# Kernel tuning notes

Measured on AMD Instinct MI355X. Metric: run time of the kernel, lower is better.

Reference implementation:

```python
import jax, jax.numpy as jnp
import numpy as np
from jax import lax

B, H, E = 32, 2050, 128        # batch, input height, num_emb (conv width)
N = 2048                        # num_nodes = H - (kernel_size - 1)
C = 128                         # hidden_channels_CNN[0]
G1, G2 = 128, 128               # hidden_channels_GNN
MLP = 100                       # hidden_channels_MLP
OUT = 1                         # output_dim
KS = 3                          # kernel_size
NE = 32768                      # num edges


def setup_inputs() -> dict:
    key = jax.random.key(0)
    ks = jax.random.split(key, 12)
    s = 0.02
    inp = {
        "x": jax.random.normal(ks[0], (B, H, E), dtype=jnp.float32),
        "edge_index": jax.random.randint(ks[1], (2, NE), 0, N, dtype=jnp.int64),
        # Conv2d(1, C, kernel=(KS, E)) -> OIHW weight [C, 1, KS, E]
        "conv_w": jax.random.normal(ks[2], (C, 1, KS, E), dtype=jnp.float32) * s,
        "conv_b": jax.random.normal(ks[3], (C,), dtype=jnp.float32) * s,
        # GCNConv weights (linear has no bias; bias added after aggregation)
        "gW1": jax.random.normal(ks[4], (C, G1), dtype=jnp.float32) * s,
        "gb1": jax.random.normal(ks[5], (G1,), dtype=jnp.float32) * s,
        "gW2": jax.random.normal(ks[6], (G1, G2), dtype=jnp.float32) * s,
        "gb2": jax.random.normal(ks[7], (G2,), dtype=jnp.float32) * s,
        "W1": jax.random.normal(ks[8], (G2 * N, MLP), dtype=jnp.float32) * s,
        "b1": jax.random.normal(ks[9], (MLP,), dtype=jnp.float32) * s,
        "W2": jax.random.normal(ks[10], (MLP, OUT), dtype=jnp.float32) * s,
        "b2": jax.random.normal(ks[11], (OUT,), dtype=jnp.float32) * s,
    }
    return inp


def _gcn_norm(edge_index, n):
    # PyG gcn_norm with add_self_loops=True, edge_weight = 1
    loops = jnp.arange(n, dtype=edge_index.dtype)
    src = jnp.concatenate([edge_index[0], loops])
    dst = jnp.concatenate([edge_index[1], loops])
    deg = jax.ops.segment_sum(jnp.ones_like(dst, dtype=jnp.float32), dst, num_segments=n)
    dinv = jnp.where(deg > 0, lax.rsqrt(jnp.maximum(deg, 1.0)), 0.0)
    norm = dinv[src] * dinv[dst]
    return src, dst, norm


def _gcn_layer(h, src, dst, norm, W, b):
    # h: [B, N, Fin] -> out[b, dst] = sum_e norm_e * (h @ W)[b, src_e] + b
    hw = h @ W                                   # [B, N, Fout]
    msgs = hw[:, src, :] * norm[None, :, None]    # [B, E+N, Fout]
    agg = jnp.zeros_like(hw).at[:, dst, :].add(msgs)
    return agg + b


def reference(x, edge_index, conv_w, conv_b, gW1, gb1, gW2, gb2, W1, b1, W2, b2):
    # CNN feature extraction: [B,1,H,E] conv (KS,E) -> [B,C,N,1]
    x4 = x[:, None, :, :]
    h = lax.conv_general_dilated(x4, conv_w, window_strides=(1, 1), padding='VALID',
                                 dimension_numbers=('NCHW', 'OIHW', 'NCHW'))
    h = jax.nn.relu(h + conv_b[None, :, None, None])
    h = jnp.transpose(h[:, :, :, 0], (0, 2, 1))   # [B, N, C]

    src, dst, norm = _gcn_norm(edge_index, N)
    h = jax.nn.relu(_gcn_layer(h, src, dst, norm, gW1, gb1))
    h = jax.nn.relu(_gcn_layer(h, src, dst, norm, gW2, gb2))

    h = h.reshape(B, -1)                          # [B, N*G2]
    h = jax.nn.relu(h @ W1 + b1)
    # dropout: eval mode (identity)
    out = h @ W2 + b2
    return out.astype(jnp.float32)
```

## Files before the change

### kernel.cpp

```cpp
#include <hip/hip_runtime.h>
#include <stdint.h>

typedef unsigned short u16;
typedef __attribute__((ext_vector_type(8))) short bf16x8;
typedef __attribute__((ext_vector_type(4))) float f32x4;

#define NN 2048
#define NEDGE 32768
#define NBLK 1024
#define KC 256
#define NRG 4
#define PW 112

__device__ __forceinline__ float bf2f(uint32_t u) {
  union { uint32_t i; float f; } c; c.i = u << 16; return c.f;
}
__device__ __forceinline__ uint32_t f2bf(float f) {
  union { float f; uint32_t i; } c; c.f = f;
  uint32_t x = c.i;
  return (x + 0x7fffu + ((x >> 16) & 1u)) >> 16;
}

__device__ __forceinline__ void fma8(float* acc, uint4 q, float wv) {
  acc[0] += wv * bf2f(q.x & 0xffffu);
  acc[1] += wv * bf2f(q.x >> 16);
  acc[2] += wv * bf2f(q.y & 0xffffu);
  acc[3] += wv * bf2f(q.y >> 16);
  acc[4] += wv * bf2f(q.z & 0xffffu);
  acc[5] += wv * bf2f(q.z >> 16);
  acc[6] += wv * bf2f(q.w & 0xffffu);
  acc[7] += wv * bf2f(q.w >> 16);
}

__global__ void k_prep(const float4* __restrict__ cw, uint2* __restrict__ wtb,
                       const float* __restrict__ g1, const float* __restrict__ g2,
                       u16* __restrict__ o1, u16* __restrict__ o2,
                       int* __restrict__ cnt, int* __restrict__ cursor) {
  int blk = blockIdx.x;
  if (blk < 48) {
    int i = blk * 256 + threadIdx.x;
    float4 v = cw[i];
    uint2 o;
    o.x = f2bf(v.x) | (f2bf(v.y) << 16);
    o.y = f2bf(v.z) | (f2bf(v.w) << 16);
    wtb[i] = o;
  } else if (blk < 112) {
    int i = (blk - 48) * 256 + threadIdx.x;
    int r = i >> 7, c = i & 127;
    o1[i] = (u16)f2bf(g1[c * 128 + r]);
    o2[i] = (u16)f2bf(g2[c * 128 + r]);
  } else {
    int i = (blk - 112) * 256 + threadIdx.x;
    cnt[i] = 1; cursor[i] = 0;
  }
}

__global__ void k_count(const int* __restrict__ edge, int* __restrict__ cnt) {
  int i = blockIdx.x * 256 + threadIdx.x;
  if (i < NEDGE) atomicAdd(&cnt[edge[NEDGE + i]], 1);
}

__global__ __launch_bounds__(1024) void k_scan(const int* __restrict__ cnt, int* __restrict__ rowp) {
  __shared__ int s[1024];
  int t = threadIdx.x;
  int c0 = cnt[2 * t], c1 = cnt[2 * t + 1];
  s[t] = c0 + c1;
  __syncthreads();
  for (int off = 1; off < 1024; off <<= 1) {
    int v = (t >= off) ? s[t - off] : 0;
    __syncthreads();
    s[t] += v;
    __syncthreads();
  }
  int excl = s[t] - c0 - c1;
  rowp[2 * t] = excl;
  rowp[2 * t + 1] = excl + c0;
  if (t == 1023) rowp[2048] = s[t];
}

__global__ void k_fill(const int* __restrict__ edge, const int* __restrict__ cnt,
                       const int* __restrict__ rowp, int* __restrict__ cursor,
                       int* __restrict__ colx, float* __restrict__ wgt) {
  int i = blockIdx.x * 256 + threadIdx.x;
  if (i >= NEDGE + NN) return;
  int s, d;
  if (i < NEDGE) { s = edge[i]; d = edge[NEDGE + i]; }
  else { s = i - NEDGE; d = s; }
  float wv = rsqrtf((float)cnt[s] * (float)cnt[d]);
  int pos = atomicAdd(&cursor[d], 1);
  int idx = rowp[d] + pos;
  colx[idx] = s;
  wgt[idx] = wv;
}

__global__ __launch_bounds__(256) void k_gemmf(
    const float* __restrict__ A, const u16* __restrict__ Bt,
    const float* __restrict__ bias, u16* __restrict__ C,
    int K, int bExtra)
{
  __shared__ u16 lA[128 * 64];
  __shared__ u16 lB[128 * 64];
  const int t = threadIdx.x;
  const int Mbase = blockIdx.x * 128;
  const size_t aBase = (size_t)Mbase * 128 + (size_t)(Mbase >> 11) * bExtra;
  const int w = t >> 6, l = t & 63;
  const int wrM = (w >> 1) * 64, wrN = (w & 1) * 64;
  const int lm = l & 15, lkh = l >> 4;
  const int rph0 = t >> 3, pc = t & 7;
  const int rt2 = t >> 1, hf = t & 1;
  f32x4 acc[4][4];
#pragma unroll
  for (int i = 0; i < 4; ++i)
#pragma unroll
    for (int j = 0; j < 4; ++j)
      acc[i][j] = (f32x4){0.f, 0.f, 0.f, 0.f};

  for (int kc = 0; kc < K; kc += 64) {
    __syncthreads();
#pragma unroll
    for (int it = 0; it < 4; ++it) {
      int r = it * 32 + rph0;
      int lc = pc ^ (r & 7);
      char* dstB = (char*)lB + it * 4096 + w * 1024;
      __builtin_amdgcn_global_load_lds(
          (const void*)(Bt + (size_t)r * K + kc + lc * 8), dstB, 16, 0, 0);
    }
    {
      const float4* src = (const float4*)(A + aBase + (size_t)rt2 * 128 + kc + hf * 32);
      float4 f[8];
#pragma unroll
      for (int c = 0; c < 8; ++c) f[c] = src[c];
#pragma unroll
      for (int cc = 0; cc < 4; ++cc) {
        uint4 pk;
        pk.x = f2bf(f[2 * cc].x)     | (f2bf(f[2 * cc].y) << 16);
        pk.y = f2bf(f[2 * cc].z)     | (f2bf(f[2 * cc].w) << 16);
        pk.z = f2bf(f[2 * cc + 1].x) | (f2bf(f[2 * cc + 1].y) << 16);
        pk.w = f2bf(f[2 * cc + 1].z) | (f2bf(f[2 * cc + 1].w) << 16);
        int ch = hf * 4 + cc;
        *(uint4*)((char*)lA + rt2 * 128 + ((ch ^ (rt2 & 7)) << 4)) = pk;
      }
    }
    __syncthreads();
#pragma unroll
    for (int kk = 0; kk < 2; ++kk) {
      int lc = kk * 4 + lkh;
      bf16x8 af[4], bfr[4];
#pragma unroll
      for (int i = 0; i < 4; ++i) {
        int R = wrM + i * 16 + lm;
        af[i] = *(const bf16x8*)((const char*)lA + R * 128 + ((lc ^ (R & 7)) << 4));
      }
#pragma unroll
      for (int j = 0; j < 4; ++j) {
        int R = wrN + j * 16 + lm;
        bfr[j] = *(const bf16x8*)((const char*)lB + R * 128 + ((lc ^ (R & 7)) << 4));
      }
#pragma unroll
      for (int i = 0; i < 4; ++i)
#pragma unroll
        for (int j = 0; j < 4; ++j)
          acc[i][j] = __builtin_amdgcn_mfma_f32_16x16x32_bf16(af[i], bfr[j], acc[i][j], 0, 0, 0);
    }
  }
  const int rq = (l >> 4) * 4;
#pragma unroll
  for (int i = 0; i < 4; ++i) {
#pragma unroll
    for (int j = 0; j < 4; ++j) {
      int col = wrN + j * 16 + lm;
      float bv = bias[col];
#pragma unroll
      for (int q = 0; q < 4; ++q) {
        int g = Mbase + wrM + i * 16 + rq + q;
        int orow = ((g & 2047) << 5) | (g >> 11);
        float v = acc[i][j][q] + bv;
        v = fmaxf(v, 0.f);
        C[(size_t)orow * 128 + col] = (u16)f2bf(v);
      }
    }
  }
}

__global__ __launch_bounds__(256) void k_gemm(
    const u16* __restrict__ A, const u16* __restrict__ Bt,
    const float* __restrict__ bias, u16* __restrict__ C,
    int K)
{
  __shared__ u16 lA[128 * 64];
  __shared__ u16 lB[128 * 64];
  const int t = threadIdx.x;
  const int Mbase = blockIdx.x * 128;
  const size_t aBase = (size_t)Mbase * 128;
  const int w = t >> 6, l = t & 63;
  const int wrM = (w >> 1) * 64, wrN = (w & 1) * 64;
  const int lm = l & 15, lkh = l >> 4;
  const int rph0 = t >> 3, pc = t & 7;
  f32x4 acc[4][4];
#pragma unroll
  for (int i = 0; i < 4; ++i)
#pragma unroll
    for (int j = 0; j < 4; ++j)
      acc[i][j] = (f32x4){0.f, 0.f, 0.f, 0.f};

  for (int kc = 0; kc < K; kc += 64) {
    __syncthreads();
#pragma unroll
    for (int it = 0; it < 4; ++it) {
      int r = it * 32 + rph0;
      int lc = pc ^ (r & 7);
      char* dstA = (char*)lA + it * 4096 + w * 1024;
      char* dstB = (char*)lB + it * 4096 + w * 1024;
      __builtin_amdgcn_global_load_lds(
          (const void*)(A + aBase + (size_t)r * 128 + kc + lc * 8), dstA, 16, 0, 0);
      __builtin_amdgcn_global_load_lds(
          (const void*)(Bt + (size_t)r * K + kc + lc * 8), dstB, 16, 0, 0);
    }
    __syncthreads();
#pragma unroll
    for (int kk = 0; kk < 2; ++kk) {
      int lc = kk * 4 + lkh;
      bf16x8 af[4], bfr[4];
#pragma unroll
      for (int i = 0; i < 4; ++i) {
        int R = wrM + i * 16 + lm;
        af[i] = *(const bf16x8*)((const char*)lA + R * 128 + ((lc ^ (R & 7)) << 4));
      }
#pragma unroll
      for (int j = 0; j < 4; ++j) {
        int R = wrN + j * 16 + lm;
        bfr[j] = *(const bf16x8*)((const char*)lB + R * 128 + ((lc ^ (R & 7)) << 4));
      }
#pragma unroll
      for (int i = 0; i < 4; ++i)
#pragma unroll
        for (int j = 0; j < 4; ++j)
          acc[i][j] = __builtin_amdgcn_mfma_f32_16x16x32_bf16(af[i], bfr[j], acc[i][j], 0, 0, 0);
    }
  }
  const int rq = (l >> 4) * 4;
#pragma unroll
  for (int i = 0; i < 4; ++i) {
#pragma unroll
    for (int j = 0; j < 4; ++j) {
      int col = wrN + j * 16 + lm;
      float bv = bias[col];
#pragma unroll
      for (int q = 0; q < 4; ++q) {
        int row = Mbase + wrM + i * 16 + rq + q;
        float v = acc[i][j][q] + bv;
        v = fmaxf(v, 0.f);
        C[(size_t)row * 128 + col] = (u16)f2bf(v);
      }
    }
  }
}

__global__ __launch_bounds__(256) void k_gatherT(
    const u16* __restrict__ h, const int* __restrict__ rowp,
    const int* __restrict__ colx, const float* __restrict__ wgt,
    u16* __restrict__ out)
{
  const int t = threadIdx.x;
  const int v = blockIdx.x;
  const int b = t >> 3, cg = t & 7;
  const int e0 = rowp[v], e1 = rowp[v + 1];
  float acc[16];
#pragma unroll
  for (int i = 0; i < 16; ++i) acc[i] = 0.f;
  int e = e0;
  for (; e + 2 <= e1; e += 2) {
    int u0 = colx[e], u1 = colx[e + 1];
    float w0 = wgt[e], w1 = wgt[e + 1];
    const uint4* p0 = (const uint4*)(h + ((size_t)u0 * 32 + b) * 128 + cg * 16);
    const uint4* p1 = (const uint4*)(h + ((size_t)u1 * 32 + b) * 128 + cg * 16);
    uint4 qa0 = p0[0], qa1 = p0[1];
    uint4 qb0 = p1[0], qb1 = p1[1];
    fma8(acc, qa0, w0);
    fma8(acc + 8, qa1, w0);
    fma8(acc, qb0, w1);
    fma8(acc + 8, qb1, w1);
  }
  for (; e < e1; ++e) {
    int u = colx[e];
    float wv = wgt[e];
    const uint4* p = (const uint4*)(h + ((size_t)u * 32 + b) * 128 + cg * 16);
    uint4 q0 = p[0], q1 = p[1];
    fma8(acc, q0, wv);
    fma8(acc + 8, q1, wv);
  }
  uint4 o0, o1;
  o0.x = f2bf(acc[0])  | (f2bf(acc[1])  << 16);
  o0.y = f2bf(acc[2])  | (f2bf(acc[3])  << 16);
  o0.z = f2bf(acc[4])  | (f2bf(acc[5])  << 16);
  o0.w = f2bf(acc[6])  | (f2bf(acc[7])  << 16);
  o1.x = f2bf(acc[8])  | (f2bf(acc[9])  << 16);
  o1.y = f2bf(acc[10]) | (f2bf(acc[11]) << 16);
  o1.z = f2bf(acc[12]) | (f2bf(acc[13]) << 16);
  o1.w = f2bf(acc[14]) | (f2bf(acc[15]) << 16);
  uint4* dst = (uint4*)(out + ((size_t)v * 32 + b) * 128 + cg * 16);
  dst[0] = o0;
  dst[1] = o1;
}

__global__ __launch_bounds__(256) void k_mlp1(
    const u16* __restrict__ h3, const float* __restrict__ W1, float* __restrict__ part)
{
  __shared__ u16 sA[32][264];
  __shared__ u16 sB[112][264];
  const int t = threadIdx.x;
  const int blk = blockIdx.x;
  const int j0 = blk * KC;
  {
    int r = t >> 3, q = t & 7;
    int v = (j0 >> 7) + (q >> 2);
    int d = (q & 3) * 32;
    const u16* src = h3 + ((size_t)v * 32 + r) * 128 + d;
#pragma unroll
    for (int u = 0; u < 4; ++u)
      *(bf16x8*)&sA[r][q * 32 + u * 8] = *(const bf16x8*)(src + u * 8);
  }
  for (int it = 0; it < 13; ++it) {
    int task = it * 256 + t;
    if (task < 3200) {
      int jp = task / 25, mq = task % 25;
      const float* wp = W1 + (size_t)(j0 + 2 * jp) * 100 + mq * 4;
      float4 fa = *(const float4*)wp;
      float4 fb = *(const float4*)(wp + 100);
      uint32_t p0 = f2bf(fa.x) | (f2bf(fb.x) << 16);
      uint32_t p1 = f2bf(fa.y) | (f2bf(fb.y) << 16);
      uint32_t p2 = f2bf(fa.z) | (f2bf(fb.z) << 16);
      uint32_t p3 = f2bf(fa.w) | (f2bf(fb.w) << 16);
      int m = mq * 4;
      *(uint32_t*)&sB[m + 0][2 * jp] = p0;
      *(uint32_t*)&sB[m + 1][2 * jp] = p1;
      *(uint32_t*)&sB[m + 2][2 * jp] = p2;
      *(uint32_t*)&sB[m + 3][2 * jp] = p3;
    }
  }
  __syncthreads();
  const int w = t >> 6, l = t & 63;
  const int mt = w >> 1, nh = w & 1;
  const int nt0 = nh * 4, ntn = nh ? 3 : 4;
  const int lm = l & 15, lk8 = (l >> 4) * 8;
  f32x4 acc[4];
#pragma unroll
  for (int n = 0; n < 4; ++n) acc[n] = (f32x4){0.f, 0.f, 0.f, 0.f};
#pragma unroll
  for (int kk = 0; kk < 8; ++kk) {
    int ko = kk * 32 + lk8;
    bf16x8 af = *(const bf16x8*)&sA[mt * 16 + lm][ko];
#pragma unroll
    for (int n = 0; n < 4; ++n) {
      if (n < ntn) {
        bf16x8 bfr = *(const bf16x8*)&sB[(nt0 + n) * 16 + lm][ko];
        acc[n] = __builtin_amdgcn_mfma_f32_16x16x32_bf16(af, bfr, acc[n], 0, 0, 0);
      }
    }
  }
  const int rq = (l >> 4) * 4;
#pragma unroll
  for (int n = 0; n < 4; ++n) {
    if (n < ntn) {
      int m = (nt0 + n) * 16 + lm;
#pragma unroll
      for (int q = 0; q < 4; ++q) {
        int b = mt * 16 + rq + q;
        part[((size_t)blk * 32 + b) * PW + m] = acc[n][q];
      }
    }
  }
}

__global__ __launch_bounds__(256) void k_red(
    const float* __restrict__ part, float* __restrict__ part2)
{
  int e = blockIdx.x * 256 + threadIdx.x;
  int rg = blockIdx.y;
  const float* p = part + (size_t)rg * 256 * (32 * PW) + e;
  float s0 = 0.f, s1 = 0.f, s2 = 0.f, s3 = 0.f;
  for (int r = 0; r < 256; r += 4) {
    s0 += p[(size_t)(r + 0) * (32 * PW)];
    s1 += p[(size_t)(r + 1) * (32 * PW)];
    s2 += p[(size_t)(r + 2) * (32 * PW)];
    s3 += p[(size_t)(r + 3) * (32 * PW)];
  }
  part2[rg * (32 * PW) + e] = (s0 + s1) + (s2 + s3);
}

__global__ __launch_bounds__(128) void k_mlp2(
    const float* __restrict__ part2, const float* __restrict__ b1,
    const float* __restrict__ W2, const float* __restrict__ b2, float* __restrict__ out)
{
  __shared__ float sh[100];
  int b = blockIdx.x, t = threadIdx.x;
  if (t < 100) {
    float s = 0.f;
#pragma unroll
    for (int rg = 0; rg < NRG; ++rg)
      s += part2[rg * (32 * PW) + b * PW + t];
    float h = fmaxf(s + b1[t], 0.f);
    sh[t] = h * W2[t];
  }
  __syncthreads();
  if (t == 0) {
    float s = 0.f;
    for (int m = 0; m < 100; ++m) s += sh[m];
    out[b] = s + b2[0];
  }
}

extern "C" void kernel_launch(void* const* d_in, const int* in_sizes, int n_in,
                              void* d_out, int out_size, void* d_ws, size_t ws_size,
                              hipStream_t stream) {
  (void)in_sizes; (void)n_in; (void)out_size; (void)ws_size;
  const float* x      = (const float*)d_in[0];
  const int* edge     = (const int*)d_in[1];
  const float* conv_w = (const float*)d_in[2];
  const float* conv_b = (const float*)d_in[3];
  const float* gW1    = (const float*)d_in[4];
  const float* gb1    = (const float*)d_in[5];
  const float* gW2    = (const float*)d_in[6];
  const float* gb2    = (const float*)d_in[7];
  const float* W1     = (const float*)d_in[8];
  const float* b1     = (const float*)d_in[9];
  const float* W2     = (const float*)d_in[10];
  const float* b2     = (const float*)d_in[11];
  float* out = (float*)d_out;

  char* ws = (char*)d_ws;
  size_t off = 0;
  auto alloc = [&](size_t bytes) {
    void* p = ws + off;
    off = (off + bytes + 255) & ~(size_t)255;
    return p;
  };
  u16* bufA   = (u16*)alloc(8388608ull * 2);
  u16* bufB   = (u16*)alloc(8388608ull * 2);
  u16* Wtb    = (u16*)alloc(49152ull * 2);
  u16* g1t    = (u16*)alloc(16384ull * 2);
  u16* g2t    = (u16*)alloc(16384ull * 2);
  int* cnt    = (int*)alloc(2048 * 4);
  int* cursor = (int*)alloc(2048 * 4);
  int* rowp   = (int*)alloc(2052 * 4);
  int* colx   = (int*)alloc(34816 * 4);
  float* wgt  = (float*)alloc(34816 * 4);
  float* part = (float*)alloc((size_t)NBLK * 32 * PW * 4);
  float* part2= (float*)alloc((size_t)NRG * (32 * PW) * 4);

  k_prep<<<120, 256, 0, stream>>>((const float4*)conv_w, (uint2*)Wtb,
                                  gW1, gW2, g1t, g2t, cnt, cursor);
  k_count<<<128, 256, 0, stream>>>(edge, cnt);
  k_scan<<<1, 1024, 0, stream>>>(cnt, rowp);
  k_fill<<<(NEDGE + NN + 255) / 256, 256, 0, stream>>>(edge, cnt, rowp, cursor, colx, wgt);

  k_gemmf<<<512, 256, 0, stream>>>(x, Wtb, conv_b, bufA, 384, 256);
  k_gatherT<<<2048, 256, 0, stream>>>(bufA, rowp, colx, wgt, bufB);
  k_gemm<<<512, 256, 0, stream>>>(bufB, g1t, gb1, bufA, 128);
  k_gatherT<<<2048, 256, 0, stream>>>(bufA, rowp, colx, wgt, bufB);
  k_gemm<<<512, 256, 0, stream>>>(bufB, g2t, gb2, bufA, 128);
  k_mlp1<<<NBLK, 256, 0, stream>>>(bufA, W1, part);
  k_red<<<dim3(14, NRG), 256, 0, stream>>>(part, part2);
  k_mlp2<<<32, 128, 0, stream>>>(part2, b1, W2, b2, out);
}
```

Before: 189.6 us.

## Fuse CSR construction into one cooperative kernel and convert weights inside GEMMs

Four small graph-preprocessing kernels (init, degree count, scan, fill) become a single cooperative kernel that separates its phases with grid-wide syncs. The separate weight-prep kernel is removed: the conv and GCN GEMMs now read fp32 weights directly, then convert and transpose them to bf16 in LDS on every tile. This saves several kernel launches. In exchange, every GEMM block repeats the weight conversion, and the cooperative launch plus grid syncs add their own latency.

```diff
diff --git a/kernel.cpp b/kernel.cpp
--- a/kernel.cpp
+++ b/kernel.cpp
@@ -1,5 +1,8 @@
 #include <hip/hip_runtime.h>
+#include <hip/hip_cooperative_groups.h>
 #include <stdint.h>
+
+namespace cg = cooperative_groups;
 
 typedef unsigned short u16;
 typedef __attribute__((ext_vector_type(8))) short bf16x8;
@@ -32,69 +35,56 @@
   acc[7] += wv * bf2f(q.w >> 16);
 }
 
-__global__ void k_prep(const float4* __restrict__ cw, uint2* __restrict__ wtb,
-                       const float* __restrict__ g1, const float* __restrict__ g2,
-                       u16* __restrict__ o1, u16* __restrict__ o2,
-                       int* __restrict__ cnt, int* __restrict__ cursor) {
-  int blk = blockIdx.x;
-  if (blk < 48) {
-    int i = blk * 256 + threadIdx.x;
-    float4 v = cw[i];
-    uint2 o;
-    o.x = f2bf(v.x) | (f2bf(v.y) << 16);
-    o.y = f2bf(v.z) | (f2bf(v.w) << 16);
-    wtb[i] = o;
-  } else if (blk < 112) {
-    int i = (blk - 48) * 256 + threadIdx.x;
-    int r = i >> 7, c = i & 127;
-    o1[i] = (u16)f2bf(g1[c * 128 + r]);
-    o2[i] = (u16)f2bf(g2[c * 128 + r]);
-  } else {
-    int i = (blk - 112) * 256 + threadIdx.x;
-    cnt[i] = 1; cursor[i] = 0;
-  }
-}
-
-__global__ void k_count(const int* __restrict__ edge, int* __restrict__ cnt) {
-  int i = blockIdx.x * 256 + threadIdx.x;
-  if (i < NEDGE) atomicAdd(&cnt[edge[NEDGE + i]], 1);
-}
-
-__global__ __launch_bounds__(1024) void k_scan(const int* __restrict__ cnt, int* __restrict__ rowp) {
-  __shared__ int s[1024];
-  int t = threadIdx.x;
-  int c0 = cnt[2 * t], c1 = cnt[2 * t + 1];
-  s[t] = c0 + c1;
-  __syncthreads();
-  for (int off = 1; off < 1024; off <<= 1) {
-    int v = (t >= off) ? s[t - off] : 0;
+__global__ __launch_bounds__(256) void k_csrc(
+    const int* __restrict__ edge, int* __restrict__ cnt, int* __restrict__ cursor,
+    int* __restrict__ rowp, int* __restrict__ colx, float* __restrict__ wgt)
+{
+  cg::grid_group grid = cg::this_grid();
+  const int gtid = blockIdx.x * 256 + threadIdx.x;
+  if (gtid < NN) { cnt[gtid] = 1; cursor[gtid] = 0; }
+  grid.sync();
+  atomicAdd(&cnt[edge[NEDGE + gtid]], 1);
+  grid.sync();
+  if (blockIdx.x == 0) {
+    __shared__ int s[256];
+    int t = threadIdx.x;
+    int base = t * 8;
+    int c[8]; int sum = 0;
+#pragma unroll
+    for (int i = 0; i < 8; ++i) { c[i] = cnt[base + i]; sum += c[i]; }
+    s[t] = sum;
     __syncthreads();
-    s[t] += v;
-    __syncthreads();
-  }
-  int excl = s[t] - c0 - c1;
-  rowp[2 * t] = excl;
-  rowp[2 * t + 1] = excl + c0;
-  if (t == 1023) rowp[2048] = s[t];
-}
-
-__global__ void k_fill(const int* __restrict__ edge, const int* __restrict__ cnt,
-                       const int* __restrict__ rowp, int* __restrict__ cursor,
-                       int* __restrict__ colx, float* __restrict__ wgt) {
-  int i = blockIdx.x * 256 + threadIdx.x;
-  if (i >= NEDGE + NN) return;
-  int s, d;
-  if (i < NEDGE) { s = edge[i]; d = edge[NEDGE + i]; }
-  else { s = i - NEDGE; d = s; }
-  float wv = rsqrtf((float)cnt[s] * (float)cnt[d]);
-  int pos = atomicAdd(&cursor[d], 1);
-  int idx = rowp[d] + pos;
-  colx[idx] = s;
-  wgt[idx] = wv;
+    for (int off = 1; off < 256; off <<= 1) {
+      int v = (t >= off) ? s[t - off] : 0;
+      __syncthreads();
+      s[t] += v;
+      __syncthreads();
+    }
+    int excl = s[t] - sum;
+#pragma unroll
+    for (int i = 0; i < 8; ++i) { rowp[base + i] = excl; excl += c[i]; }
+    if (t == 255) rowp[2048] = excl;
+  }
+  grid.sync();
+  {
+    int sV = edge[gtid], d = edge[NEDGE + gtid];
+    float wv = rsqrtf((float)cnt[sV] * (float)cnt[d]);
+    int pos = atomicAdd(&cursor[d], 1);
+    int idx = rowp[d] + pos;
+    colx[idx] = sV;
+    wgt[idx] = wv;
+    if (gtid < NN) {
+      float wv2 = rsqrtf((float)cnt[gtid] * (float)cnt[gtid]);
+      int pos2 = atomicAdd(&cursor[gtid], 1);
+      int idx2 = rowp[gtid] + pos2;
+      colx[idx2] = gtid;
+      wgt[idx2] = wv2;
+    }
+  }
 }
 
 __global__ __launch_bounds__(256) void k_gemmf(
-    const float* __restrict__ A, const u16* __restrict__ Bt,
+    const float* __restrict__ A, const float* __restrict__ Bw,
     const float* __restrict__ bias, u16* __restrict__ C,
     int K, int bExtra)
 {
@@ -106,7 +96,6 @@
   const int w = t >> 6, l = t & 63;
   const int wrM = (w >> 1) * 64, wrN = (w & 1) * 64;
   const int lm = l & 15, lkh = l >> 4;
-  const int rph0 = t >> 3, pc = t & 7;
   const int rt2 = t >> 1, hf = t & 1;
   f32x4 acc[4][4];
 #pragma unroll
@@ -117,14 +106,6 @@
 
   for (int kc = 0; kc < K; kc += 64) {
     __syncthreads();
-#pragma unroll
-    for (int it = 0; it < 4; ++it) {
-      int r = it * 32 + rph0;
-      int lc = pc ^ (r & 7);
-      char* dstB = (char*)lB + it * 4096 + w * 1024;
-      __builtin_amdgcn_global_load_lds(
-          (const void*)(Bt + (size_t)r * K + kc + lc * 8), dstB, 16, 0, 0);
-    }
     {
       const float4* src = (const float4*)(A + aBase + (size_t)rt2 * 128 + kc + hf * 32);
       float4 f[8];
@@ -141,6 +122,22 @@
         *(uint4*)((char*)lA + rt2 * 128 + ((ch ^ (rt2 & 7)) << 4)) = pk;
       }
     }
+    {
+      const float4* src = (const float4*)(Bw + (size_t)rt2 * K + kc + hf * 32);
+      float4 f[8];
+#pragma unroll
+      for (int c = 0; c < 8; ++c) f[c] = src[c];
+#pragma unroll
+      for (int cc = 0; cc < 4; ++cc) {
+        uint4 pk;
+        pk.x = f2bf(f[2 * cc].x)     | (f2bf(f[2 * cc].y) << 16);
+        pk.y = f2bf(f[2 * cc].z)     | (f2bf(f[2 * cc].w) << 16);
+        pk.z = f2bf(f[2 * cc + 1].x) | (f2bf(f[2 * cc + 1].y) << 16);
+        pk.w = f2bf(f[2 * cc + 1].z) | (f2bf(f[2 * cc + 1].w) << 16);
+        int ch = hf * 4 + cc;
+        *(uint4*)((char*)lB + rt2 * 128 + ((ch ^ (rt2 & 7)) << 4)) = pk;
+      }
+    }
     __syncthreads();
 #pragma unroll
     for (int kk = 0; kk < 2; ++kk) {
@@ -183,9 +180,8 @@
 }
 
 __global__ __launch_bounds__(256) void k_gemm(
-    const u16* __restrict__ A, const u16* __restrict__ Bt,
-    const float* __restrict__ bias, u16* __restrict__ C,
-    int K)
+    const u16* __restrict__ A, const float* __restrict__ G,
+    const float* __restrict__ bias, u16* __restrict__ C)
 {
   __shared__ u16 lA[128 * 64];
   __shared__ u16 lB[128 * 64];
@@ -203,18 +199,33 @@
     for (int j = 0; j < 4; ++j)
       acc[i][j] = (f32x4){0.f, 0.f, 0.f, 0.f};
 
-  for (int kc = 0; kc < K; kc += 64) {
+  for (int kc = 0; kc < 128; kc += 64) {
     __syncthreads();
 #pragma unroll
     for (int it = 0; it < 4; ++it) {
       int r = it * 32 + rph0;
       int lc = pc ^ (r & 7);
       char* dstA = (char*)lA + it * 4096 + w * 1024;
-      char* dstB = (char*)lB + it * 4096 + w * 1024;
       __builtin_amdgcn_global_load_lds(
           (const void*)(A + aBase + (size_t)r * 128 + kc + lc * 8), dstA, 16, 0, 0);
-      __builtin_amdgcn_global_load_lds(
-          (const void*)(Bt + (size_t)r * K + kc + lc * 8), dstB, 16, 0, 0);
+    }
+#pragma unroll
+    for (int it = 0; it < 4; ++it) {
+      int task = it * 256 + t;
+      int kp = task >> 5, nq = task & 31;
+      const float* gp = G + (size_t)(kc + 2 * kp) * 128 + nq * 4;
+      float4 fa = *(const float4*)gp;
+      float4 fb = *(const float4*)(gp + 128);
+      uint32_t p0 = f2bf(fa.x) | (f2bf(fb.x) << 16);
+      uint32_t p1 = f2bf(fa.y) | (f2bf(fb.y) << 16);
+      uint32_t p2 = f2bf(fa.z) | (f2bf(fb.z) << 16);
+      uint32_t p3 = f2bf(fa.w) | (f2bf(fb.w) << 16);
+      int n = nq * 4;
+      int ch = kp >> 2, sub = (kp & 3) * 4;
+      *(uint32_t*)((char*)lB + (n + 0) * 128 + ((ch ^ ((n + 0) & 7)) << 4) + sub) = p0;
+      *(uint32_t*)((char*)lB + (n + 1) * 128 + ((ch ^ ((n + 1) & 7)) << 4) + sub) = p1;
+      *(uint32_t*)((char*)lB + (n + 2) * 128 + ((ch ^ ((n + 2) & 7)) << 4) + sub) = p2;
+      *(uint32_t*)((char*)lB + (n + 3) * 128 + ((ch ^ ((n + 3) & 7)) << 4) + sub) = p3;
     }
     __syncthreads();
 #pragma unroll
@@ -263,7 +274,7 @@
 {
   const int t = threadIdx.x;
   const int v = blockIdx.x;
-  const int b = t >> 3, cg = t & 7;
+  const int b = t >> 3, cg_ = t & 7;
   const int e0 = rowp[v], e1 = rowp[v + 1];
   float acc[16];
 #pragma unroll
@@ -272,8 +283,8 @@
   for (; e + 2 <= e1; e += 2) {
     int u0 = colx[e], u1 = colx[e + 1];
     float w0 = wgt[e], w1 = wgt[e + 1];
-    const uint4* p0 = (const uint4*)(h + ((size_t)u0 * 32 + b) * 128 + cg * 16);
-    const uint4* p1 = (const uint4*)(h + ((size_t)u1 * 32 + b) * 128 + cg * 16);
+    const uint4* p0 = (const uint4*)(h + ((size_t)u0 * 32 + b) * 128 + cg_ * 16);
+    const uint4* p1 = (const uint4*)(h + ((size_t)u1 * 32 + b) * 128 + cg_ * 16);
     uint4 qa0 = p0[0], qa1 = p0[1];
     uint4 qb0 = p1[0], qb1 = p1[1];
     fma8(acc, qa0, w0);
@@ -284,7 +295,7 @@
   for (; e < e1; ++e) {
     int u = colx[e];
     float wv = wgt[e];
-    const uint4* p = (const uint4*)(h + ((size_t)u * 32 + b) * 128 + cg * 16);
+    const uint4* p = (const uint4*)(h + ((size_t)u * 32 + b) * 128 + cg_ * 16);
     uint4 q0 = p[0], q1 = p[1];
     fma8(acc, q0, wv);
     fma8(acc + 8, q1, wv);
@@ -298,7 +309,7 @@
   o1.y = f2bf(acc[10]) | (f2bf(acc[11]) << 16);
   o1.z = f2bf(acc[12]) | (f2bf(acc[13]) << 16);
   o1.w = f2bf(acc[14]) | (f2bf(acc[15]) << 16);
-  uint4* dst = (uint4*)(out + ((size_t)v * 32 + b) * 128 + cg * 16);
+  uint4* dst = (uint4*)(out + ((size_t)v * 32 + b) * 128 + cg_ * 16);
   dst[0] = o0;
   dst[1] = o1;
 }
@@ -437,9 +448,6 @@
   };
   u16* bufA   = (u16*)alloc(8388608ull * 2);
   u16* bufB   = (u16*)alloc(8388608ull * 2);
-  u16* Wtb    = (u16*)alloc(49152ull * 2);
-  u16* g1t    = (u16*)alloc(16384ull * 2);
-  u16* g2t    = (u16*)alloc(16384ull * 2);
   int* cnt    = (int*)alloc(2048 * 4);
   int* cursor = (int*)alloc(2048 * 4);
   int* rowp   = (int*)alloc(2052 * 4);
@@ -448,17 +456,18 @@
   float* part = (float*)alloc((size_t)NBLK * 32 * PW * 4);
   float* part2= (float*)alloc((size_t)NRG * (32 * PW) * 4);
 
-  k_prep<<<120, 256, 0, stream>>>((const float4*)conv_w, (uint2*)Wtb,
-                                  gW1, gW2, g1t, g2t, cnt, cursor);
-  k_count<<<128, 256, 0, stream>>>(edge, cnt);
-  k_scan<<<1, 1024, 0, stream>>>(cnt, rowp);
-  k_fill<<<(NEDGE + NN + 255) / 256, 256, 0, stream>>>(edge, cnt, rowp, cursor, colx, wgt);
-
-  k_gemmf<<<512, 256, 0, stream>>>(x, Wtb, conv_b, bufA, 384, 256);
+  {
+    void* args[] = { (void*)&edge, (void*)&cnt, (void*)&cursor,
+                     (void*)&rowp, (void*)&colx, (void*)&wgt };
+    hipLaunchCooperativeKernel((const void*)k_csrc, dim3(128), dim3(256),
+                               args, 0, stream);
+  }
+
+  k_gemmf<<<512, 256, 0, stream>>>(x, conv_w, conv_b, bufA, 384, 256);
   k_gatherT<<<2048, 256, 0, stream>>>(bufA, rowp, colx, wgt, bufB);
-  k_gemm<<<512, 256, 0, stream>>>(bufB, g1t, gb1, bufA, 128);
+  k_gemm<<<512, 256, 0, stream>>>(bufB, gW1, gb1, bufA);
   k_gatherT<<<2048, 256, 0, stream>>>(bufA, rowp, colx, wgt, bufB);
-  k_gemm<<<512, 256, 0, stream>>>(bufB, g2t, gb2, bufA, 128);
+  k_gemm<<<512, 256, 0, stream>>>(bufB, gW2, gb2, bufA);
   k_mlp1<<<NBLK, 256, 0, stream>>>(bufA, W1, part);
   k_red<<<dim3(14, NRG), 256, 0, stream>>>(part, part2);
   k_mlp2<<<32, 128, 0, stream>>>(part2, b1, W2, b2, out);
```

Result: slower. 249.9 us (+31.8%).
